# Performance work log

Hardware: AMD Instinct MI355X
Metric: run time of the kernel (lower is better)

The kernel has to match this reference:

```python
import jax, jax.numpy as jnp
import numpy as np

BN_EPS = 1e-5  # torch BatchNorm1d default


def setup_inputs() -> dict:
    key = jax.random.key(0)
    k = jax.random.split(key, 5)
    B, D, L = 4096, 4096, 4  # batch, width, num layers (3 hidden + 1 output)
    x = jax.random.normal(k[0], (B, D), dtype=jnp.float32)
    # Per-layer Linear weights stored as [L, in, out]; scaled like xavier-ish init.
    W = jax.random.normal(k[1], (L, D, D), dtype=jnp.float32) * (1.0 / np.sqrt(D))
    b = jax.random.normal(k[2], (L, D), dtype=jnp.float32) * 0.01
    gamma = jax.random.uniform(k[3], (L, D), dtype=jnp.float32, minval=0.5, maxval=1.5)
    beta = jax.random.normal(k[4], (L, D), dtype=jnp.float32) * 0.1
    return {"x": x, "W": W, "b": b, "gamma": gamma, "beta": beta}


def _layer(h, W_l, b_l, gamma_l, beta_l):
    # one big GEMM replaces the per-neuron GEMV loop + stack
    h = h @ W_l + b_l  # [B, out]
    # BatchNorm1d, training mode: biased batch stats over the batch dim
    mu = jnp.mean(h, axis=0)
    var = jnp.var(h, axis=0)
    h = (h - mu) * jax.lax.rsqrt(var + BN_EPS) * gamma_l + beta_l
    return jax.nn.relu(h)


def reference(x, W, b, gamma, beta):
    out = x
    for l in range(W.shape[0]):  # small fixed layer count
        out = _layer(out, W[l], b[l], gamma[l], beta[l])
    # nn.Softmax(dim=0): softmax over the batch dimension, as in the original
    return jax.nn.softmax(out, axis=0)
```

## Files before the change

### kernel.cpp

```cpp
#include <hip/hip_runtime.h>
#include <stdint.h>

#define DIMD 4096
#define DIMB 4096
#define NLAYER 4
#define NT (DIMD / 64)

typedef unsigned short u16;
typedef __attribute__((ext_vector_type(4))) float f32x4;
typedef __attribute__((ext_vector_type(8))) __bf16 bf16x8;

__device__ __forceinline__ u16 f2bf(float f) {
    union { float f; uint32_t u; } v; v.f = f;
    return (u16)((v.u + 0x7fffu + ((v.u >> 16) & 1u)) >> 16);
}

__global__ void k_cvt(const float* __restrict__ in, u16* __restrict__ out) {
    int i = (blockIdx.x * 256 + threadIdx.x) * 4;
    float4 v = *reinterpret_cast<const float4*>(in + i);
    ushort4 r;
    r.x = f2bf(v.x); r.y = f2bf(v.y); r.z = f2bf(v.z); r.w = f2bf(v.w);
    *reinterpret_cast<ushort4*>(out + i) = r;
}

__global__ void k_trans(const float* __restrict__ W, u16* __restrict__ Wt) {
    __shared__ float tile[64][65];
    const int t = threadIdx.x;
    const size_t loff = (size_t)blockIdx.z * DIMD * DIMD;
    const int n0 = blockIdx.x * 64, k0 = blockIdx.y * 64;
    const int kr = t >> 4, c4 = (t & 15) * 4;
    #pragma unroll
    for (int r = 0; r < 4; ++r) {
        float4 v = *reinterpret_cast<const float4*>(W + loff + (size_t)(k0 + kr + r * 16) * DIMD + n0 + c4);
        tile[kr + r * 16][c4 + 0] = v.x;
        tile[kr + r * 16][c4 + 1] = v.y;
        tile[kr + r * 16][c4 + 2] = v.z;
        tile[kr + r * 16][c4 + 3] = v.w;
    }
    __syncthreads();
    const int nr = t >> 4, k4 = (t & 15) * 4;
    #pragma unroll
    for (int r = 0; r < 4; ++r) {
        int n = nr + r * 16;
        ushort4 o;
        o.x = f2bf(tile[k4 + 0][n]);
        o.y = f2bf(tile[k4 + 1][n]);
        o.z = f2bf(tile[k4 + 2][n]);
        o.w = f2bf(tile[k4 + 3][n]);
        *reinterpret_cast<ushort4*>(Wt + loff + (size_t)(n0 + n) * DIMD + k0 + k4) = o;
    }
}

#define GLD(g, l) __builtin_amdgcn_global_load_lds( \
    (__attribute__((address_space(1))) void*)(g),   \
    (__attribute__((address_space(3))) void*)(l), 16, 0, 0)

__global__ __launch_bounds__(512, 2) void k_gemm(
        const u16* __restrict__ A, const u16* __restrict__ Bt,
        const float* __restrict__ bias, float* __restrict__ C,
        float* __restrict__ csum, float* __restrict__ csum2) {
    __shared__ __attribute__((aligned(16))) u16 As[2 * 256 * 64];
    __shared__ __attribute__((aligned(16))) u16 Bs[2 * 256 * 64];
    const int tid = threadIdx.x;
    const int lane = tid & 63, wv = tid >> 6;
    const int wm = wv >> 2, wn = wv & 3;
    const int bm = blockIdx.y, bn = blockIdx.x;
    const int lr = lane & 15, lk = lane >> 4;

    const int r0 = tid >> 3;
    const int cswz = (tid & 7) ^ (r0 & 7);
    const u16* gA = A  + (size_t)(bm * 256 + r0) * DIMD + cswz * 8;
    const u16* gB = Bt + (size_t)(bn * 256 + r0) * DIMD + cswz * 8;

#define STAGE_A(h, t, buf) do { \
    const u16* _s = gA + (size_t)(h) * 128 * DIMD + (size_t)(t) * 64; \
    u16* _d = As + (buf) * 16384 + (h) * 8192 + wv * 512; \
    GLD(_s, _d); GLD(_s + (size_t)64 * DIMD, _d + 4096); \
} while (0)
#define STAGE_B(h, t, buf) do { \
    const u16* _s = gB + (size_t)(h) * 128 * DIMD + (size_t)(t) * 64; \
    u16* _d = Bs + (buf) * 16384 + (h) * 8192 + wv * 512; \
    GLD(_s, _d); GLD(_s + (size_t)64 * DIMD, _d + 4096); \
} while (0)

    int aoff[4][2], boff[2][2];
    #pragma unroll
    for (int mf = 0; mf < 4; ++mf)
        #pragma unroll
        for (int ks = 0; ks < 2; ++ks) {
            int row = wm * 128 + mf * 16 + lr;
            aoff[mf][ks] = row * 64 + ((ks * 4 + lk) ^ (row & 7)) * 8;
        }
    #pragma unroll
    for (int nf = 0; nf < 2; ++nf)
        #pragma unroll
        for (int ks = 0; ks < 2; ++ks) {
            int row = wn * 64 + nf * 16 + lr;
            boff[nf][ks] = row * 64 + ((ks * 4 + lk) ^ (row & 7)) * 8;
        }

    f32x4 acc[8][4] = {};
    bf16x8 al[4][2], ah[4][2], b0[2][2], b1[2][2];

    STAGE_B(0, 0, 0); STAGE_B(1, 0, 0); STAGE_A(0, 0, 0); STAGE_A(1, 0, 0);
    STAGE_B(0, 1, 1); STAGE_B(1, 1, 1); STAGE_A(0, 1, 1); STAGE_A(1, 1, 1);
    asm volatile("s_waitcnt vmcnt(8)" ::: "memory");
    __builtin_amdgcn_s_barrier();

    for (int t = 0; t < NT; ++t) {
        const int cur = t & 1;
        const u16* Ab = As + cur * 16384;
        const u16* Bb = Bs + cur * 16384;
        const bool pf = (t + 2 < NT);

        #pragma unroll
        for (int mf = 0; mf < 4; ++mf)
            #pragma unroll
            for (int ks = 0; ks < 2; ++ks)
                al[mf][ks] = *reinterpret_cast<const bf16x8*>(Ab + aoff[mf][ks]);
        #pragma unroll
        for (int nf = 0; nf < 2; ++nf)
            #pragma unroll
            for (int ks = 0; ks < 2; ++ks)
                b0[nf][ks] = *reinterpret_cast<const bf16x8*>(Bb + boff[nf][ks]);
        #pragma unroll
        for (int nf = 0; nf < 2; ++nf)
            #pragma unroll
            for (int ks = 0; ks < 2; ++ks)
                b1[nf][ks] = *reinterpret_cast<const bf16x8*>(Bb + 2048 + boff[nf][ks]);

        __builtin_amdgcn_s_setprio(1);
        #pragma unroll
        for (int mf = 0; mf < 4; ++mf)
            #pragma unroll
            for (int nf = 0; nf < 2; ++nf)
                #pragma unroll
                for (int ks = 0; ks < 2; ++ks)
                    acc[mf][nf] = __builtin_amdgcn_mfma_f32_16x16x32_bf16(
                        al[mf][ks], b0[nf][ks], acc[mf][nf], 0, 0, 0);
        __builtin_amdgcn_s_setprio(0);

        #pragma unroll
        for (int mf = 0; mf < 4; ++mf)
            #pragma unroll
            for (int ks = 0; ks < 2; ++ks)
                ah[mf][ks] = *reinterpret_cast<const bf16x8*>(Ab + 4096 + aoff[mf][ks]);

        __builtin_amdgcn_s_setprio(1);
        #pragma unroll
        for (int mf = 0; mf < 4; ++mf)
            #pragma unroll
            for (int nf = 0; nf < 2; ++nf)
                #pragma unroll
                for (int ks = 0; ks < 2; ++ks)
                    acc[mf][2 + nf] = __builtin_amdgcn_mfma_f32_16x16x32_bf16(
                        al[mf][ks], b1[nf][ks], acc[mf][2 + nf], 0, 0, 0);
        __builtin_amdgcn_s_setprio(0);

        asm volatile("s_waitcnt lgkmcnt(0)" ::: "memory");
        __builtin_amdgcn_sched_barrier(0);
        __builtin_amdgcn_s_barrier();

        if (pf) {
            STAGE_B(0, t + 2, cur); STAGE_B(1, t + 2, cur);
            STAGE_A(0, t + 2, cur); STAGE_A(1, t + 2, cur);
        }

        __builtin_amdgcn_s_setprio(1);
        #pragma unroll
        for (int mf = 0; mf < 4; ++mf)
            #pragma unroll
            for (int nf = 0; nf < 2; ++nf)
                #pragma unroll
                for (int ks = 0; ks < 2; ++ks)
                    acc[4 + mf][2 + nf] = __builtin_amdgcn_mfma_f32_16x16x32_bf16(
                        ah[mf][ks], b1[nf][ks], acc[4 + mf][2 + nf], 0, 0, 0);
        #pragma unroll
        for (int mf = 0; mf < 4; ++mf)
            #pragma unroll
            for (int nf = 0; nf < 2; ++nf)
                #pragma unroll
                for (int ks = 0; ks < 2; ++ks)
                    acc[4 + mf][nf] = __builtin_amdgcn_mfma_f32_16x16x32_bf16(
                        ah[mf][ks], b0[nf][ks], acc[4 + mf][nf], 0, 0, 0);
        __builtin_amdgcn_s_setprio(0);

        if (pf) asm volatile("s_waitcnt vmcnt(8)" ::: "memory");
        else    asm volatile("s_waitcnt vmcnt(0)" ::: "memory");
        __builtin_amdgcn_s_barrier();
    }

    #pragma unroll
    for (int nh = 0; nh < 2; ++nh)
        #pragma unroll
        for (int nf = 0; nf < 2; ++nf) {
            int n = nh * 2 + nf;
            int col = bn * 256 + wn * 64 + nh * 32 + nf * 16 + lr;
            float bv = bias[col];
            float s1 = 0.f, s2 = 0.f;
            #pragma unroll
            for (int m = 0; m < 8; ++m) {
                int rbase = bm * 256 + wm * 128 + (m >> 2) * 64 + (m & 3) * 16 + lk * 4;
                #pragma unroll
                for (int r = 0; r < 4; ++r) {
                    float v = acc[m][n][r] + bv;
                    C[(size_t)(rbase + r) * DIMD + col] = v;
                    s1 += v; s2 += v * v;
                }
            }
            s1 += __shfl_xor(s1, 16); s1 += __shfl_xor(s1, 32);
            s2 += __shfl_xor(s2, 16); s2 += __shfl_xor(s2, 32);
            if (lk == 0) {
                atomicAdd(&csum[col], s1);
                atomicAdd(&csum2[col], s2);
            }
        }
#undef STAGE_A
#undef STAGE_B
}

__global__ void k_norm(const float* __restrict__ H, const float* __restrict__ sum,
                       const float* __restrict__ sum2, const float* __restrict__ gamma,
                       const float* __restrict__ beta, u16* __restrict__ o) {
    int j = (blockIdx.x * 256 + threadIdx.x) * 4;
    int i0 = blockIdx.y * 128;
    float4 sm = *reinterpret_cast<const float4*>(sum + j);
    float4 s2 = *reinterpret_cast<const float4*>(sum2 + j);
    float4 gm = *reinterpret_cast<const float4*>(gamma + j);
    float4 bt = *reinterpret_cast<const float4*>(beta + j);
    float s[4], tt[4];
    #pragma unroll
    for (int c = 0; c < 4; ++c) {
        float mu = (&sm.x)[c] * (1.0f / DIMB);
        float var = (&s2.x)[c] * (1.0f / DIMB) - mu * mu;
        s[c] = (&gm.x)[c] * rsqrtf(var + 1e-5f);
        tt[c] = (&bt.x)[c] - mu * s[c];
    }
    for (int i = i0; i < i0 + 128; ++i) {
        float4 h = *reinterpret_cast<const float4*>(H + (size_t)i * DIMD + j);
        ushort4 r;
        #pragma unroll
        for (int c = 0; c < 4; ++c)
            (&r.x)[c] = f2bf(fmaxf((&h.x)[c] * s[c] + tt[c], 0.0f));
        *reinterpret_cast<ushort4*>(o + (size_t)i * DIMD + j) = r;
    }
}

__global__ void k_normexp(float* __restrict__ H, const float* __restrict__ sum,
                          const float* __restrict__ sum2, const float* __restrict__ gamma,
                          const float* __restrict__ beta, float* __restrict__ esum) {
    int j = (blockIdx.x * 256 + threadIdx.x) * 4;
    int i0 = blockIdx.y * 128;
    float4 sm = *reinterpret_cast<const float4*>(sum + j);
    float4 s2 = *reinterpret_cast<const float4*>(sum2 + j);
    float4 gm = *reinterpret_cast<const float4*>(gamma + j);
    float4 bt = *reinterpret_cast<const float4*>(beta + j);
    float s[4], tt[4], acc[4] = {0.f, 0.f, 0.f, 0.f};
    #pragma unroll
    for (int c = 0; c < 4; ++c) {
        float mu = (&sm.x)[c] * (1.0f / DIMB);
        float var = (&s2.x)[c] * (1.0f / DIMB) - mu * mu;
        s[c] = (&gm.x)[c] * rsqrtf(var + 1e-5f);
        tt[c] = (&bt.x)[c] - mu * s[c];
    }
    for (int i = i0; i < i0 + 128; ++i) {
        float4 h = *reinterpret_cast<const float4*>(H + (size_t)i * DIMD + j);
        #pragma unroll
        for (int c = 0; c < 4; ++c) {
            float e = __expf(fmaxf((&h.x)[c] * s[c] + tt[c], 0.0f));
            (&h.x)[c] = e;
            acc[c] += e;
        }
        *reinterpret_cast<float4*>(H + (size_t)i * DIMD + j) = h;
    }
    #pragma unroll
    for (int c = 0; c < 4; ++c) atomicAdd(&esum[j + c], acc[c]);
}

__global__ void k_div(float* __restrict__ H, const float* __restrict__ esum) {
    int i = (blockIdx.x * 256 + threadIdx.x) * 4;
    float4 v = *reinterpret_cast<const float4*>(H + i);
    const float4 e = *reinterpret_cast<const float4*>(esum + (i & (DIMD - 1)));
    v.x /= e.x; v.y /= e.y; v.z /= e.z; v.w /= e.w;
    *reinterpret_cast<float4*>(H + i) = v;
}

extern "C" void kernel_launch(void* const* d_in, const int* in_sizes, int n_in,
                              void* d_out, int out_size, void* d_ws, size_t ws_size,
                              hipStream_t stream) {
    (void)in_sizes; (void)n_in; (void)out_size; (void)ws_size;
    const float* x     = (const float*)d_in[0];
    const float* W     = (const float*)d_in[1];
    const float* b     = (const float*)d_in[2];
    const float* gamma = (const float*)d_in[3];
    const float* beta  = (const float*)d_in[4];
    float* out = (float*)d_out;

    char* ws = (char*)d_ws;
    u16*  Abf = (u16*)ws;
    u16*  Wt4 = (u16*)(ws + (size_t)32 * 1024 * 1024);
    float* stats = (float*)(ws + (size_t)160 * 1024 * 1024);
    hipMemsetAsync(stats, 0, (4 * 8192 + 4096) * sizeof(float), stream);

    k_cvt<<<DIMB * DIMD / 1024, 256, 0, stream>>>(x, Abf);
    k_trans<<<dim3(64, 64, 4), 256, 0, stream>>>(W, Wt4);

    for (int l = 0; l < NLAYER; ++l) {
        float* sum = stats + l * 8192;
        float* sum2 = sum + 4096;
        k_gemm<<<dim3(16, 16), 512, 0, stream>>>(Abf, Wt4 + (size_t)l * DIMD * DIMD,
                                                 b + l * DIMD, out, sum, sum2);
        if (l < NLAYER - 1)
            k_norm<<<dim3(4, 32), 256, 0, stream>>>(out, sum, sum2,
                gamma + l * DIMD, beta + l * DIMD, Abf);
        else
            k_normexp<<<dim3(4, 32), 256, 0, stream>>>(out, sum, sum2,
                gamma + l * DIMD, beta + l * DIMD, stats + 32768);
    }
    k_div<<<DIMB * DIMD / 1024, 256, 0, stream>>>(out, stats + 32768);
}
```

Baseline: 793.4 us.

## Switch GEMM main loop to K=32 tiles with four-stage LDS ring buffer

The GEMM K-loop now works on 32-wide K slices instead of 64 and keeps a four-deep LDS ring, prefetching three tiles ahead with a single barrier per iteration. The old split A/B fragment loading and the interleaved half-tile MFMA phases are replaced by one flat 8x4 MFMA block per step, with a new XOR swizzle for the 32-element rows. The aim is deeper latency hiding for the global-to-LDS loads and fewer barriers per unit of work. The cost is twice as many loop iterations, with less compute between barriers and more loop overhead.

After: 996.6 us. 25.6% more time.

```diff
diff --git a/kernel.cpp b/kernel.cpp
--- a/kernel.cpp
+++ b/kernel.cpp
@@ -4,7 +4,7 @@
 #define DIMD 4096
 #define DIMB 4096
 #define NLAYER 4
-#define NT (DIMD / 64)
+#define NT2 128
 
 typedef unsigned short u16;
 typedef __attribute__((ext_vector_type(4))) float f32x4;
@@ -59,164 +59,103 @@
         const u16* __restrict__ A, const u16* __restrict__ Bt,
         const float* __restrict__ bias, float* __restrict__ C,
         float* __restrict__ csum, float* __restrict__ csum2) {
-    __shared__ __attribute__((aligned(16))) u16 As[2 * 256 * 64];
-    __shared__ __attribute__((aligned(16))) u16 Bs[2 * 256 * 64];
+    __shared__ __attribute__((aligned(16))) u16 As[4 * 8192];
+    __shared__ __attribute__((aligned(16))) u16 Bs[4 * 8192];
     const int tid = threadIdx.x;
     const int lane = tid & 63, wv = tid >> 6;
     const int wm = wv >> 2, wn = wv & 3;
     const int bm = blockIdx.y, bn = blockIdx.x;
     const int lr = lane & 15, lk = lane >> 4;
 
-    const int r0 = tid >> 3;
-    const int cswz = (tid & 7) ^ (r0 & 7);
+    const int r0 = tid >> 2;
+    const int cswz = (tid & 3) ^ ((r0 >> 1) & 3);
     const u16* gA = A  + (size_t)(bm * 256 + r0) * DIMD + cswz * 8;
     const u16* gB = Bt + (size_t)(bn * 256 + r0) * DIMD + cswz * 8;
 
-#define STAGE_A(h, t, buf) do { \
-    const u16* _s = gA + (size_t)(h) * 128 * DIMD + (size_t)(t) * 64; \
-    u16* _d = As + (buf) * 16384 + (h) * 8192 + wv * 512; \
-    GLD(_s, _d); GLD(_s + (size_t)64 * DIMD, _d + 4096); \
+#define STG_A(t) do { \
+    const u16* _s = gA + (size_t)(t) * 32; \
+    u16* _d = As + (((t) & 3) * 8192) + wv * 512; \
+    GLD(_s, _d); GLD(_s + (size_t)128 * DIMD, _d + 4096); \
 } while (0)
-#define STAGE_B(h, t, buf) do { \
-    const u16* _s = gB + (size_t)(h) * 128 * DIMD + (size_t)(t) * 64; \
-    u16* _d = Bs + (buf) * 16384 + (h) * 8192 + wv * 512; \
-    GLD(_s, _d); GLD(_s + (size_t)64 * DIMD, _d + 4096); \
+#define STG_B(t) do { \
+    const u16* _s = gB + (size_t)(t) * 32; \
+    u16* _d = Bs + (((t) & 3) * 8192) + wv * 512; \
+    GLD(_s, _d); GLD(_s + (size_t)128 * DIMD, _d + 4096); \
 } while (0)
 
-    int aoff[4][2], boff[2][2];
-    #pragma unroll
-    for (int mf = 0; mf < 4; ++mf)
-        #pragma unroll
-        for (int ks = 0; ks < 2; ++ks) {
-            int row = wm * 128 + mf * 16 + lr;
-            aoff[mf][ks] = row * 64 + ((ks * 4 + lk) ^ (row & 7)) * 8;
-        }
-    #pragma unroll
-    for (int nf = 0; nf < 2; ++nf)
-        #pragma unroll
-        for (int ks = 0; ks < 2; ++ks) {
-            int row = wn * 64 + nf * 16 + lr;
-            boff[nf][ks] = row * 64 + ((ks * 4 + lk) ^ (row & 7)) * 8;
-        }
+    int aoff[8], boff[4];
+    #pragma unroll
+    for (int mf = 0; mf < 8; ++mf) {
+        int row = wm * 128 + mf * 16 + lr;
+        aoff[mf] = row * 32 + ((lk ^ ((row >> 1) & 3)) << 3);
+    }
+    #pragma unroll
+    for (int nf = 0; nf < 4; ++nf) {
+        int row = wn * 64 + nf * 16 + lr;
+        boff[nf] = row * 32 + ((lk ^ ((row >> 1) & 3)) << 3);
+    }
 
     f32x4 acc[8][4] = {};
-    bf16x8 al[4][2], ah[4][2], b0[2][2], b1[2][2];
-
-    STAGE_B(0, 0, 0); STAGE_B(1, 0, 0); STAGE_A(0, 0, 0); STAGE_A(1, 0, 0);
-    STAGE_B(0, 1, 1); STAGE_B(1, 1, 1); STAGE_A(0, 1, 1); STAGE_A(1, 1, 1);
+    bf16x8 a[8], b[4];
+
+    STG_A(0); STG_B(0); STG_A(1); STG_B(1); STG_A(2); STG_B(2);
     asm volatile("s_waitcnt vmcnt(8)" ::: "memory");
     __builtin_amdgcn_s_barrier();
 
-    for (int t = 0; t < NT; ++t) {
-        const int cur = t & 1;
-        const u16* Ab = As + cur * 16384;
-        const u16* Bb = Bs + cur * 16384;
-        const bool pf = (t + 2 < NT);
-
-        #pragma unroll
-        for (int mf = 0; mf < 4; ++mf)
+    for (int t = 0; t < NT2; ++t) {
+        const u16* Ab = As + (t & 3) * 8192;
+        const u16* Bb = Bs + (t & 3) * 8192;
+
+        if (t + 3 < NT2) { STG_A(t + 3); STG_B(t + 3); }
+
+        #pragma unroll
+        for (int nf = 0; nf < 4; ++nf)
+            b[nf] = *reinterpret_cast<const bf16x8*>(Bb + boff[nf]);
+        #pragma unroll
+        for (int mf = 0; mf < 8; ++mf)
+            a[mf] = *reinterpret_cast<const bf16x8*>(Ab + aoff[mf]);
+
+        __builtin_amdgcn_s_setprio(1);
+        #pragma unroll
+        for (int mf = 0; mf < 8; ++mf)
             #pragma unroll
-            for (int ks = 0; ks < 2; ++ks)
-                al[mf][ks] = *reinterpret_cast<const bf16x8*>(Ab + aoff[mf][ks]);
-        #pragma unroll
-        for (int nf = 0; nf < 2; ++nf)
-            #pragma unroll
-            for (int ks = 0; ks < 2; ++ks)
-                b0[nf][ks] = *reinterpret_cast<const bf16x8*>(Bb + boff[nf][ks]);
-        #pragma unroll
-        for (int nf = 0; nf < 2; ++nf)
-            #pragma unroll
-            for (int ks = 0; ks < 2; ++ks)
-                b1[nf][ks] = *reinterpret_cast<const bf16x8*>(Bb + 2048 + boff[nf][ks]);
-
-        __builtin_amdgcn_s_setprio(1);
-        #pragma unroll
-        for (int mf = 0; mf < 4; ++mf)
-            #pragma unroll
-            for (int nf = 0; nf < 2; ++nf)
-                #pragma unroll
-                for (int ks = 0; ks < 2; ++ks)
-                    acc[mf][nf] = __builtin_amdgcn_mfma_f32_16x16x32_bf16(
-                        al[mf][ks], b0[nf][ks], acc[mf][nf], 0, 0, 0);
-        __builtin_amdgcn_s_setprio(0);
-
-        #pragma unroll
-        for (int mf = 0; mf < 4; ++mf)
-            #pragma unroll
-            for (int ks = 0; ks < 2; ++ks)
-                ah[mf][ks] = *reinterpret_cast<const bf16x8*>(Ab + 4096 + aoff[mf][ks]);
-
-        __builtin_amdgcn_s_setprio(1);
-        #pragma unroll
-        for (int mf = 0; mf < 4; ++mf)
-            #pragma unroll
-            for (int nf = 0; nf < 2; ++nf)
-                #pragma unroll
-                for (int ks = 0; ks < 2; ++ks)
-                    acc[mf][2 + nf] = __builtin_amdgcn_mfma_f32_16x16x32_bf16(
-                        al[mf][ks], b1[nf][ks], acc[mf][2 + nf], 0, 0, 0);
+            for (int nf = 0; nf < 4; ++nf)
+                acc[mf][nf] = __builtin_amdgcn_mfma_f32_16x16x32_bf16(
+                    a[mf], b[nf], acc[mf][nf], 0, 0, 0);
         __builtin_amdgcn_s_setprio(0);
 
         asm volatile("s_waitcnt lgkmcnt(0)" ::: "memory");
         __builtin_amdgcn_sched_barrier(0);
+        if (t + 3 < NT2)      asm volatile("s_waitcnt vmcnt(8)" ::: "memory");
+        else if (t + 2 < NT2) asm volatile("s_waitcnt vmcnt(4)" ::: "memory");
+        else                  asm volatile("s_waitcnt vmcnt(0)" ::: "memory");
         __builtin_amdgcn_s_barrier();
-
-        if (pf) {
-            STAGE_B(0, t + 2, cur); STAGE_B(1, t + 2, cur);
-            STAGE_A(0, t + 2, cur); STAGE_A(1, t + 2, cur);
-        }
-
-        __builtin_amdgcn_s_setprio(1);
-        #pragma unroll
-        for (int mf = 0; mf < 4; ++mf)
+    }
+
+    #pragma unroll
+    for (int nf = 0; nf < 4; ++nf) {
+        int col = bn * 256 + wn * 64 + nf * 16 + lr;
+        float bv = bias[col];
+        float s1 = 0.f, s2 = 0.f;
+        #pragma unroll
+        for (int mf = 0; mf < 8; ++mf) {
+            int rbase = bm * 256 + wm * 128 + mf * 16 + lk * 4;
             #pragma unroll
-            for (int nf = 0; nf < 2; ++nf)
-                #pragma unroll
-                for (int ks = 0; ks < 2; ++ks)
-                    acc[4 + mf][2 + nf] = __builtin_amdgcn_mfma_f32_16x16x32_bf16(
-                        ah[mf][ks], b1[nf][ks], acc[4 + mf][2 + nf], 0, 0, 0);
-        #pragma unroll
-        for (int mf = 0; mf < 4; ++mf)
-            #pragma unroll
-            for (int nf = 0; nf < 2; ++nf)
-                #pragma unroll
-                for (int ks = 0; ks < 2; ++ks)
-                    acc[4 + mf][nf] = __builtin_amdgcn_mfma_f32_16x16x32_bf16(
-                        ah[mf][ks], b0[nf][ks], acc[4 + mf][nf], 0, 0, 0);
-        __builtin_amdgcn_s_setprio(0);
-
-        if (pf) asm volatile("s_waitcnt vmcnt(8)" ::: "memory");
-        else    asm volatile("s_waitcnt vmcnt(0)" ::: "memory");
-        __builtin_amdgcn_s_barrier();
-    }
-
-    #pragma unroll
-    for (int nh = 0; nh < 2; ++nh)
-        #pragma unroll
-        for (int nf = 0; nf < 2; ++nf) {
-            int n = nh * 2 + nf;
-            int col = bn * 256 + wn * 64 + nh * 32 + nf * 16 + lr;
-            float bv = bias[col];
-            float s1 = 0.f, s2 = 0.f;
-            #pragma unroll
-            for (int m = 0; m < 8; ++m) {
-                int rbase = bm * 256 + wm * 128 + (m >> 2) * 64 + (m & 3) * 16 + lk * 4;
-                #pragma unroll
-                for (int r = 0; r < 4; ++r) {
-                    float v = acc[m][n][r] + bv;
-                    C[(size_t)(rbase + r) * DIMD + col] = v;
-                    s1 += v; s2 += v * v;
-                }
-            }
-            s1 += __shfl_xor(s1, 16); s1 += __shfl_xor(s1, 32);
-            s2 += __shfl_xor(s2, 16); s2 += __shfl_xor(s2, 32);
-            if (lk == 0) {
-                atomicAdd(&csum[col], s1);
-                atomicAdd(&csum2[col], s2);
+            for (int r = 0; r < 4; ++r) {
+                float v = acc[mf][nf][r] + bv;
+                C[(size_t)(rbase + r) * DIMD + col] = v;
+                s1 += v; s2 += v * v;
             }
         }
-#undef STAGE_A
-#undef STAGE_B
+        s1 += __shfl_xor(s1, 16); s1 += __shfl_xor(s1, 32);
+        s2 += __shfl_xor(s2, 16); s2 += __shfl_xor(s2, 32);
+        if (lk == 0) {
+            atomicAdd(&csum[col], s1);
+            atomicAdd(&csum2[col], s2);
+        }
+    }
+#undef STG_A
+#undef STG_B
 }
 
 __global__ void k_norm(const float* __restrict__ H, const float* __restrict__ sum,
```
